# Kernel tuning notes

Measured on AMD Instinct MI355X. Metric: run time of the kernel, lower is better.

## Reference

```python
import jax, jax.numpy as jnp
import numpy as np

DIM = 2048
N_HEADS = 16
HEAD_DIM = DIM // N_HEADS

def setup_inputs() -> dict:
    key = jax.random.key(0)
    kx, kqkv, kout = jax.random.split(key, 3)
    x = jax.random.normal(kx, (2, 2048, DIM), dtype=jnp.float32)
    # nn.Linear weights stored [out_features, in_features]; y = x @ W.T
    W_qkv = jax.random.normal(kqkv, (3 * DIM, DIM), dtype=jnp.float32) * (DIM ** -0.5)
    W_out = jax.random.normal(kout, (DIM, DIM), dtype=jnp.float32) * (DIM ** -0.5)
    return {"x": x, "W_qkv": W_qkv, "W_out": W_out}

def reference(x, W_qkv, W_out):
    B, T, D = x.shape
    qkv = jnp.einsum('btd,ed->bte', x, W_qkv)  # [B,T,3D]
    q, k, v = jnp.split(qkv, 3, axis=-1)
    def heads(t):
        return t.reshape(B, T, N_HEADS, HEAD_DIM).transpose(0, 2, 1, 3)  # [B,H,T,d]
    q, k, v = heads(q), heads(k), heads(v)
    att = jnp.einsum('bhid,bhjd->bhij', q, k) / (HEAD_DIM ** 0.5)
    causal = jnp.tril(jnp.ones((T, T), dtype=bool))
    att = jnp.where(causal, att, -jnp.inf)
    att = jax.nn.softmax(att, axis=-1)
    out = jnp.einsum('bhij,bhjd->bhid', att, v)
    out = out.transpose(0, 2, 1, 3).reshape(B, T, D)
    return jnp.einsum('btd,ed->bte', out, W_out)
```

## Files before the change

### kernel.cpp

```cpp
#include <hip/hip_runtime.h>

typedef short short8 __attribute__((ext_vector_type(8)));
typedef short short4v __attribute__((ext_vector_type(4)));
typedef float f32x4 __attribute__((ext_vector_type(4)));
typedef unsigned short u16;
typedef u16 ushort4v __attribute__((ext_vector_type(4)));

__device__ inline u16 f2bf(float f){
  unsigned int u = __builtin_bit_cast(unsigned int, f);
  u = (u + 0x7fffu + ((u >> 16) & 1u)) >> 16;
  return (u16)u;
}

__device__ inline short8 cat8(short4v a, short4v b){
  short8 r;
  r[0]=a[0]; r[1]=a[1]; r[2]=a[2]; r[3]=a[3];
  r[4]=b[0]; r[5]=b[1]; r[6]=b[2]; r[7]=b[3];
  return r;
}

__device__ inline void gload_lds16(const void* g, unsigned lds_addr){
  __builtin_amdgcn_global_load_lds((__attribute__((address_space(1))) void*)(uintptr_t)g,
                                   (__attribute__((address_space(3))) void*)(uintptr_t)lds_addr,
                                   16, 0, 0);
}

__global__ void cvt_bf16(const float* __restrict__ in, u16* __restrict__ out, int n4){
  int stride = gridDim.x * blockDim.x;
  for (int i = blockIdx.x * blockDim.x + threadIdx.x; i < n4; i += stride){
    float4 v = ((const float4*)in)[i];
    ushort4v r = { f2bf(v.x), f2bf(v.y), f2bf(v.z), f2bf(v.w) };
    ((ushort4v*)out)[i] = r;
  }
}

template<int OUT_BF16>
__global__ __launch_bounds__(256) void gemm_bt(const u16* __restrict__ A, const u16* __restrict__ B,
                                               void* __restrict__ Cv, int M, int N, int K){
  __shared__ u16 As[128 * 64];
  __shared__ u16 Bs[128 * 64];
  const int tid  = threadIdx.x;
  const int wave = tid >> 6, lane = tid & 63;
  const int lr = lane & 15, lg = lane >> 4;
  const int wm = wave >> 1, wn = wave & 1;
  const long bm = blockIdx.x * 128L, bn = blockIdx.y * 128L;
  const unsigned asb = (unsigned)(uintptr_t)As;
  const unsigned bsb = (unsigned)(uintptr_t)Bs;

  const int  srow = wave * 32 + (lane >> 3);
  const int  scol = ((lane & 7) ^ (lane >> 3)) * 8;
  const u16* aptr = A + (bm + srow) * (long)K + scol;
  const u16* bptr = B + (bn + srow) * (long)K + scol;
  const unsigned sdst = (unsigned)(wave * 4096);

  f32x4 acc[4][4] = {};
  for (int k0 = 0; k0 < K; k0 += 64){
    #pragma unroll
    for (int c = 0; c < 4; c++){
      gload_lds16(aptr + (size_t)(8 * c) * K + k0, asb + sdst + 1024u * c);
      gload_lds16(bptr + (size_t)(8 * c) * K + k0, bsb + sdst + 1024u * c);
    }
    __syncthreads();
    #pragma unroll
    for (int kk = 0; kk < 2; kk++){
      short8 af[4], bfr[4];
      #pragma unroll
      for (int m = 0; m < 4; m++){
        int row = wm * 64 + m * 16 + lr;
        int phys = (kk * 4 + lg) ^ (row & 7);
        af[m] = *(const short8*)&As[row * 64 + phys * 8];
      }
      #pragma unroll
      for (int n = 0; n < 4; n++){
        int row = wn * 64 + n * 16 + lr;
        int phys = (kk * 4 + lg) ^ (row & 7);
        bfr[n] = *(const short8*)&Bs[row * 64 + phys * 8];
      }
      #pragma unroll
      for (int m = 0; m < 4; m++)
        #pragma unroll
        for (int n = 0; n < 4; n++)
          acc[m][n] = __builtin_amdgcn_mfma_f32_16x16x32_bf16(af[m], bfr[n], acc[m][n], 0, 0, 0);
    }
    __syncthreads();
  }
  #pragma unroll
  for (int m = 0; m < 4; m++){
    #pragma unroll
    for (int n = 0; n < 4; n++){
      #pragma unroll
      for (int r = 0; r < 4; r++){
        long row = bm + wm*64 + m*16 + lg*4 + r;
        long col = bn + wn*64 + n*16 + lr;
        float v = acc[m][n][r];
        if (OUT_BF16) ((u16*)Cv)[row * (long)N + col] = f2bf(v);
        else          ((float*)Cv)[row * (long)N + col] = v;
      }
    }
  }
}

__global__ __launch_bounds__(512, 2) void attn_fwd(const u16* __restrict__ qkv, u16* __restrict__ out){
  const int T = 2048, D3 = 6144, D = 2048, HD = 128;
  const int bh = blockIdx.x;
  const int pr = blockIdx.y;
  const int b = bh >> 4, h = bh & 15;
  const int tid = threadIdx.x, wave = tid >> 6, lane = tid & 63;
  const int lr = lane & 15, lg = lane >> 4;

  __shared__ u16 Klds[64][136];
  __shared__ u16 Vlds[64][136];
  __shared__ u16 Plds[8][16][72];

  const size_t base = (size_t)b * T * D3;
  const unsigned vtr = (unsigned)(uintptr_t)&Vlds[(lane >> 4) * 8 + ((lane >> 2) & 3)][(lane & 3) * 4];

  const int srow = tid >> 4;
  const int scol = (tid & 15) * 8;
  const u16* kgp = qkv + base + (size_t)srow * D3 + D + h * HD + scol;
  const u16* vgp = kgp + D;

  for (int half = 0; half < 2; half++){
    const int qt = half ? pr : (15 - pr);
    const int q0 = qt * 128;
    const int q0w = q0 + wave * 16;

    short8 qf[4];
    {
      const u16* qrow = qkv + base + (size_t)(q0w + lr) * D3 + h * HD;
      #pragma unroll
      for (int kk = 0; kk < 4; kk++)
        qf[kk] = *(const short8*)(qrow + kk*32 + lg*8);
    }

    f32x4 o[8] = {};
    float mrow[4], lrw[4];
    #pragma unroll
    for (int r = 0; r < 4; r++){ mrow[r] = -1e30f; lrw[r] = 0.f; }

    const int ntiles = (q0 + 128) >> 6;
    short8 kreg[2], vreg[2];
    #pragma unroll
    for (int c = 0; c < 2; c++){
      kreg[c] = *(const short8*)(kgp + (size_t)(32 * c) * D3);
      vreg[c] = *(const short8*)(vgp + (size_t)(32 * c) * D3);
    }

    for (int t = 0; t < ntiles; t++){
      const int k0 = t * 64;
      __syncthreads();
      #pragma unroll
      for (int c = 0; c < 2; c++){
        *(short8*)&Klds[srow + 32*c][scol] = kreg[c];
        *(short8*)&Vlds[srow + 32*c][scol] = vreg[c];
      }
      __syncthreads();
      if (t + 1 < ntiles){
        const u16* kn = kgp + (size_t)(k0 + 64) * D3;
        const u16* vn = vgp + (size_t)(k0 + 64) * D3;
        #pragma unroll
        for (int c = 0; c < 2; c++){
          kreg[c] = *(const short8*)(kn + (size_t)(32 * c) * D3);
          vreg[c] = *(const short8*)(vn + (size_t)(32 * c) * D3);
        }
      }

      if (k0 <= q0w + 15){
        f32x4 s[4] = {};
        #pragma unroll
        for (int kh = 0; kh < 4; kh++){
          #pragma unroll
          for (int kk = 0; kk < 4; kk++){
            short8 kfrag = *(const short8*)&Klds[kh*16 + lr][kk*32 + lg*8];
            s[kh] = __builtin_amdgcn_mfma_f32_16x16x32_bf16(qf[kk], kfrag, s[kh], 0, 0, 0);
          }
        }
        const float scale = 0.08838834764831845f;
        const bool need_mask = (k0 + 63 > q0w);
        #pragma unroll
        for (int kh = 0; kh < 4; kh++){
          int key = k0 + kh*16 + lr;
          #pragma unroll
          for (int r = 0; r < 4; r++){
            float v = s[kh][r] * scale;
            if (need_mask && key > q0w + lg*4 + r) v = -1e30f;
            s[kh][r] = v;
          }
        }
        float fs[4];
        #pragma unroll
        for (int r = 0; r < 4; r++){
          float mx = fmaxf(fmaxf(s[0][r], s[1][r]), fmaxf(s[2][r], s[3][r]));
          #pragma unroll
          for (int msk = 8; msk >= 1; msk >>= 1)
            mx = fmaxf(mx, __shfl_xor(mx, msk, 64));
          float mnew = fmaxf(mrow[r], mx);
          float f = __expf(mrow[r] - mnew);
          float p0 = __expf(s[0][r] - mnew);
          float p1 = __expf(s[1][r] - mnew);
          float p2 = __expf(s[2][r] - mnew);
          float p3 = __expf(s[3][r] - mnew);
          s[0][r] = p0; s[1][r] = p1; s[2][r] = p2; s[3][r] = p3;
          float rs = (p0 + p1) + (p2 + p3);
          #pragma unroll
          for (int msk = 8; msk >= 1; msk >>= 1)
            rs += __shfl_xor(rs, msk, 64);
          lrw[r] = lrw[r] * f + rs;
          mrow[r] = mnew;
          fs[r] = f;
        }
        #pragma unroll
        for (int dt = 0; dt < 8; dt++)
          #pragma unroll
          for (int r = 0; r < 4; r++)
            o[dt][r] *= fs[r];
        #pragma unroll
        for (int kh = 0; kh < 4; kh++)
          #pragma unroll
          for (int r = 0; r < 4; r++)
            Plds[wave][lg*4 + r][kh*16 + lr] = f2bf(s[kh][r]);
        asm volatile("s_waitcnt lgkmcnt(0)" ::: "memory");
        __builtin_amdgcn_sched_barrier(0);
        short8 pf[2];
        #pragma unroll
        for (int kp2 = 0; kp2 < 2; kp2++)
          pf[kp2] = *(const short8*)&Plds[wave][lr][kp2*32 + lg*8];
        asm volatile("s_waitcnt lgkmcnt(0)" ::: "memory");
        __builtin_amdgcn_sched_barrier(0);

        short4v vf[2][2][2];
        #define TR4(BUF, PTR) \
          asm volatile("ds_read_b64_tr_b16 %0, %1"             : "=v"(vf[BUF][0][0]) : "v"(PTR)); \
          asm volatile("ds_read_b64_tr_b16 %0, %1 offset:1088" : "=v"(vf[BUF][0][1]) : "v"(PTR)); \
          asm volatile("ds_read_b64_tr_b16 %0, %1 offset:8704" : "=v"(vf[BUF][1][0]) : "v"(PTR)); \
          asm volatile("ds_read_b64_tr_b16 %0, %1 offset:9792" : "=v"(vf[BUF][1][1]) : "v"(PTR));
        TR4(0, vtr)
        #pragma unroll
        for (int dt = 0; dt < 8; dt++){
          if (dt < 7){
            unsigned pn = vtr + (unsigned)((dt + 1) * 32);
            TR4((dt + 1) & 1, pn)
            asm volatile("s_waitcnt lgkmcnt(4)" ::: "memory");
          } else {
            asm volatile("s_waitcnt lgkmcnt(0)" ::: "memory");
          }
          __builtin_amdgcn_sched_barrier(0);
          short8 v0 = cat8(vf[dt & 1][0][0], vf[dt & 1][0][1]);
          short8 v1 = cat8(vf[dt & 1][1][0], vf[dt & 1][1][1]);
          o[dt] = __builtin_amdgcn_mfma_f32_16x16x32_bf16(pf[0], v0, o[dt], 0, 0, 0);
          o[dt] = __builtin_amdgcn_mfma_f32_16x16x32_bf16(pf[1], v1, o[dt], 0, 0, 0);
        }
        #undef TR4
      }
    }
    float rl[4];
    #pragma unroll
    for (int r = 0; r < 4; r++) rl[r] = 1.0f / lrw[r];
    #pragma unroll
    for (int dt = 0; dt < 8; dt++){
      #pragma unroll
      for (int r = 0; r < 4; r++){
        float v = o[dt][r] * rl[r];
        int qa = q0w + lg*4 + r;
        out[(size_t)(b * T + qa) * D + h * HD + dt*16 + lr] = f2bf(v);
      }
    }
  }
}

extern "C" void kernel_launch(void* const* d_in, const int* in_sizes, int n_in,
                              void* d_out, int out_size, void* d_ws, size_t ws_size,
                              hipStream_t stream) {
  const float* x    = (const float*)d_in[0];
  const float* wqkv = (const float*)d_in[1];
  const float* wout = (const float*)d_in[2];
  float* out = (float*)d_out;

  u16* ws    = (u16*)d_ws;
  u16* xb    = ws;
  u16* wqkvb = xb + 8388608;
  u16* qkvb  = wqkvb + 12582912;
  u16* attnb = xb;
  u16* woutb = wqkvb;

  cvt_bf16<<<2048, 256, 0, stream>>>(x,    xb,    8388608 / 4);
  cvt_bf16<<<2048, 256, 0, stream>>>(wqkv, wqkvb, 12582912 / 4);

  gemm_bt<1><<<dim3(32, 48), 256, 0, stream>>>(xb, wqkvb, qkvb, 4096, 6144, 2048);

  cvt_bf16<<<2048, 256, 0, stream>>>(wout, woutb, 4194304 / 4);

  attn_fwd<<<dim3(32, 8), 512, 0, stream>>>(qkvb, attnb);

  gemm_bt<0><<<dim3(32, 16), 256, 0, stream>>>(attnb, woutb, out, 4096, 2048, 2048);
}
```

Before: 275.6 us.

## Double-buffer GEMM LDS loads with larger 128x256 tiles and 8 waves

Replaces the single-buffered 128x128 GEMM with a 512-thread, 128x256-tile kernel that prefetches the next K-slice into a second LDS buffer while computing the current one. Explicit vmcnt waits and barriers replace __syncthreads, and MFMA issue is wrapped in raised wave priority. This aims to hide global-to-LDS latency and raise reuse of the A tile. In exchange it uses 96KB of LDS per block and launches fewer blocks, which may reduce occupancy and leave the grid less balanced across CUs.

New measurement: 268.5 us. 2.6% less time.

```diff
diff --git a/kernel.cpp b/kernel.cpp
--- a/kernel.cpp
+++ b/kernel.cpp
@@ -35,55 +35,87 @@
 }
 
 template<int OUT_BF16>
-__global__ __launch_bounds__(256) void gemm_bt(const u16* __restrict__ A, const u16* __restrict__ B,
-                                               void* __restrict__ Cv, int M, int N, int K){
-  __shared__ u16 As[128 * 64];
-  __shared__ u16 Bs[128 * 64];
-  const int tid  = threadIdx.x;
-  const int wave = tid >> 6, lane = tid & 63;
+__global__ __launch_bounds__(512, 2) void gemm_bt2(const u16* __restrict__ A, const u16* __restrict__ B,
+                                                   void* __restrict__ Cv, int M, int N, int K){
+  __shared__ u16 lds[2][24576];
+  const int tid = threadIdx.x, wave = tid >> 6, lane = tid & 63;
   const int lr = lane & 15, lg = lane >> 4;
-  const int wm = wave >> 1, wn = wave & 1;
-  const long bm = blockIdx.x * 128L, bn = blockIdx.y * 128L;
-  const unsigned asb = (unsigned)(uintptr_t)As;
-  const unsigned bsb = (unsigned)(uintptr_t)Bs;
-
-  const int  srow = wave * 32 + (lane >> 3);
-  const int  scol = ((lane & 7) ^ (lane >> 3)) * 8;
-  const u16* aptr = A + (bm + srow) * (long)K + scol;
-  const u16* bptr = B + (bn + srow) * (long)K + scol;
-  const unsigned sdst = (unsigned)(wave * 4096);
+  const int wm = wave >> 2, wn = wave & 3;
+  const long bm = blockIdx.x * 128L, bn = blockIdx.y * 256L;
+  const int l3 = lane >> 3, l7 = lane & 7;
+
+  const u16* asrc = A + (bm + wave * 8 + l3) * (long)K + (l7 ^ l3) * 8;
+  const u16* bsrc = B + (bn + wave * 8 + l3) * (long)K + (l7 ^ l3) * 8;
+  const unsigned ldsbase = (unsigned)(uintptr_t)&lds[0][0];
+  const unsigned adst = wave * 1024u;
+  const unsigned bdst = 16384u + wave * 1024u;
+
+  #define STAGE(BUF, K0) { \
+    unsigned bb = ldsbase + (unsigned)(BUF) * 49152u; \
+    gload_lds16(asrc + (K0),                       bb + adst); \
+    gload_lds16(asrc + 64 * (size_t)K + (K0),      bb + adst + 8192u); \
+    gload_lds16(bsrc + (K0),                       bb + bdst); \
+    gload_lds16(bsrc + 64 * (size_t)K + (K0),      bb + bdst + 8192u); \
+    gload_lds16(bsrc + 128 * (size_t)K + (K0),     bb + bdst + 16384u); \
+    gload_lds16(bsrc + 192 * (size_t)K + (K0),     bb + bdst + 24576u); \
+  }
 
   f32x4 acc[4][4] = {};
-  for (int k0 = 0; k0 < K; k0 += 64){
-    #pragma unroll
-    for (int c = 0; c < 4; c++){
-      gload_lds16(aptr + (size_t)(8 * c) * K + k0, asb + sdst + 1024u * c);
-      gload_lds16(bptr + (size_t)(8 * c) * K + k0, bsb + sdst + 1024u * c);
-    }
-    __syncthreads();
+  const int nk = K >> 6;
+  int cur = 0;
+
+  STAGE(0, 0)
+  asm volatile("s_waitcnt vmcnt(0)" ::: "memory");
+  __builtin_amdgcn_sched_barrier(0);
+  __builtin_amdgcn_s_barrier();
+  __builtin_amdgcn_sched_barrier(0);
+
+  for (int t = 0; t < nk; ++t){
+    if (t + 1 < nk){
+      STAGE(cur ^ 1, (t + 1) * 64)
+      asm volatile("s_waitcnt vmcnt(6)" ::: "memory");
+    } else {
+      asm volatile("s_waitcnt vmcnt(0)" ::: "memory");
+    }
+    __builtin_amdgcn_sched_barrier(0);
+    __builtin_amdgcn_s_barrier();
+    __builtin_amdgcn_sched_barrier(0);
+
+    const u16* Ab = &lds[cur][0];
+    const u16* Bb = &lds[cur][8192];
+    short8 af[2][4], bfr[2][4];
     #pragma unroll
     for (int kk = 0; kk < 2; kk++){
-      short8 af[4], bfr[4];
       #pragma unroll
       for (int m = 0; m < 4; m++){
         int row = wm * 64 + m * 16 + lr;
         int phys = (kk * 4 + lg) ^ (row & 7);
-        af[m] = *(const short8*)&As[row * 64 + phys * 8];
+        af[kk][m] = *(const short8*)&Ab[row * 64 + phys * 8];
       }
       #pragma unroll
       for (int n = 0; n < 4; n++){
         int row = wn * 64 + n * 16 + lr;
         int phys = (kk * 4 + lg) ^ (row & 7);
-        bfr[n] = *(const short8*)&Bs[row * 64 + phys * 8];
-      }
-      #pragma unroll
-      for (int m = 0; m < 4; m++)
-        #pragma unroll
-        for (int n = 0; n < 4; n++)
-          acc[m][n] = __builtin_amdgcn_mfma_f32_16x16x32_bf16(af[m], bfr[n], acc[m][n], 0, 0, 0);
-    }
-    __syncthreads();
-  }
+        bfr[kk][n] = *(const short8*)&Bb[row * 64 + phys * 8];
+      }
+    }
+    __builtin_amdgcn_s_setprio(1);
+    #pragma unroll
+    for (int m = 0; m < 4; m++)
+      #pragma unroll
+      for (int n = 0; n < 4; n++){
+        acc[m][n] = __builtin_amdgcn_mfma_f32_16x16x32_bf16(af[0][m], bfr[0][n], acc[m][n], 0, 0, 0);
+        acc[m][n] = __builtin_amdgcn_mfma_f32_16x16x32_bf16(af[1][m], bfr[1][n], acc[m][n], 0, 0, 0);
+      }
+    __builtin_amdgcn_s_setprio(0);
+
+    __builtin_amdgcn_sched_barrier(0);
+    __builtin_amdgcn_s_barrier();
+    __builtin_amdgcn_sched_barrier(0);
+    cur ^= 1;
+  }
+  #undef STAGE
+
   #pragma unroll
   for (int m = 0; m < 4; m++){
     #pragma unroll
@@ -286,11 +318,11 @@
   cvt_bf16<<<2048, 256, 0, stream>>>(x,    xb,    8388608 / 4);
   cvt_bf16<<<2048, 256, 0, stream>>>(wqkv, wqkvb, 12582912 / 4);
 
-  gemm_bt<1><<<dim3(32, 48), 256, 0, stream>>>(xb, wqkvb, qkvb, 4096, 6144, 2048);
+  gemm_bt2<1><<<dim3(32, 24), 512, 0, stream>>>(xb, wqkvb, qkvb, 4096, 6144, 2048);
 
   cvt_bf16<<<2048, 256, 0, stream>>>(wout, woutb, 4194304 / 4);
 
   attn_fwd<<<dim3(32, 8), 512, 0, stream>>>(qkvb, attnb);
 
-  gemm_bt<0><<<dim3(32, 16), 256, 0, stream>>>(attnb, woutb, out, 4096, 2048, 2048);
-}
+  gemm_bt2<0><<<dim3(32, 8), 512, 0, stream>>>(attnb, woutb, out, 4096, 2048, 2048);
+}
```
